# Kernel optimization log

Measured on AMD Instinct MI355X. Metric: run time of the kernel, lower is better.

Reference implementation:

```python
import jax, jax.numpy as jnp
import numpy as np

S, B, C, H, W_SP = 2, 16, 256, 64, 64
K = 3

def setup_inputs() -> dict:
    key = jax.random.key(0)
    k1, k2 = jax.random.split(key)
    x = jax.random.normal(k1, (S, B, C, H, W_SP), dtype=jnp.float32)
    W = jax.random.normal(k2, (C, C, K, K), dtype=jnp.float32) * 0.05
    return {"x": x, "W": W}

def reference(x, W):
    shape = x.shape
    C_ = shape[-3]
    k = W.shape[-1]
    pad = k // 2
    # flatten leading dims -> (N, C, H, W)
    xf = x.reshape((-1,) + shape[-3:])
    # diagonal mask: zero out all cross-channel filters (effectively depthwise)
    eye = jnp.eye(C_, dtype=W.dtype)[:, :, None, None]
    w = W * eye
    out = jax.lax.conv_general_dilated(
        xf, w,
        window_strides=(1, 1),
        padding=[(pad, pad), (pad, pad)],
        dimension_numbers=("NCHW", "OIHW", "NCHW"),
    )
    return out.reshape(shape)
```

## Files before the change

kernel.cpp:

```cpp
#include <hip/hip_runtime.h>


#define C_CH 256
#define H_SP 64
#define W_SP 64
#define PLANE (H_SP * W_SP)

__global__ __launch_bounds__(256) void dwconv3x3_kernel(
    const float* __restrict__ x,
    const float* __restrict__ Wfull,
    float* __restrict__ out)
{
    __shared__ float tile[PLANE];

    const int p = blockIdx.x;
    const int c = p & (C_CH - 1);
    const float* __restrict__ xp = x + (size_t)p * PLANE;
    float* __restrict__ op = out + (size_t)p * PLANE;

    const float* __restrict__ wp = Wfull + (size_t)c * (C_CH + 1) * 9;
    const float w00 = wp[0], w01 = wp[1], w02 = wp[2];
    const float w10 = wp[3], w11 = wp[4], w12 = wp[5];
    const float w20 = wp[6], w21 = wp[7], w22 = wp[8];

    const int t = threadIdx.x;

    const float4* __restrict__ xv = (const float4*)xp;
    float4* tv = (float4*)tile;
#pragma unroll
    for (int i = 0; i < 4; ++i) {
        tv[t + i * 256] = xv[t + i * 256];
    }
    __syncthreads();

#pragma unroll
    for (int i = 0; i < 4; ++i) {
        const int f  = t + i * 256;
        const int h  = f >> 4;
        const int w4 = (f & 15) << 2;

        float4 acc = make_float4(0.f, 0.f, 0.f, 0.f);

#pragma unroll
        for (int kh = 0; kh < 3; ++kh) {
            const int hh = h + kh - 1;
            if (hh < 0 || hh >= H_SP) continue;
            const float* row = &tile[hh * W_SP];

            const float cm1 = (w4 > 0)         ? row[w4 - 1] : 0.f;
            const float c0  = row[w4];
            const float c1  = row[w4 + 1];
            const float c2  = row[w4 + 2];
            const float c3  = row[w4 + 3];
            const float c4  = (w4 + 4 < W_SP)  ? row[w4 + 4] : 0.f;

            float k0, k1, k2;
            if (kh == 0)      { k0 = w00; k1 = w01; k2 = w02; }
            else if (kh == 1) { k0 = w10; k1 = w11; k2 = w12; }
            else              { k0 = w20; k1 = w21; k2 = w22; }

            acc.x += cm1 * k0 + c0 * k1 + c1 * k2;
            acc.y += c0  * k0 + c1 * k1 + c2 * k2;
            acc.z += c1  * k0 + c2 * k1 + c3 * k2;
            acc.w += c2  * k0 + c3 * k1 + c4 * k2;
        }

        ((float4*)op)[f] = acc;
    }
}

extern "C" void kernel_launch(void* const* d_in, const int* in_sizes, int n_in,
                              void* d_out, int out_size, void* d_ws, size_t ws_size,
                              hipStream_t stream) {
    const float* x = (const float*)d_in[0];
    const float* W = (const float*)d_in[1];
    float* out = (float*)d_out;

    const int n_planes = out_size / PLANE;
    dwconv3x3_kernel<<<n_planes, 256, 0, stream>>>(x, W, out);
}
```

Measured before the change: 229.9 us.

## Replace shared-memory tile with per-wavefront register sliding window and shuffles

Each wavefront now processes a whole plane: lanes own 4-column strips of 16 rows and slide a three-row register window down their rows, getting left and right halo values through lane shuffles instead of shared memory. This drops the 16KB LDS tile and the block barrier, which removes LDS traffic and raises occupancy. In exchange, rows at strip boundaries are reloaded from global memory (about 1.125x reads), and the loads are row-strided per lane rather than fully coalesced per block. The problem is memory-bound, so the gain depends on latency hiding.

```diff
diff --git a/kernel.cpp b/kernel.cpp
--- a/kernel.cpp
+++ b/kernel.cpp
@@ -6,66 +6,78 @@
 #define W_SP 64
 #define PLANE (H_SP * W_SP)
 
-__global__ __launch_bounds__(256) void dwconv3x3_kernel(
+__global__ __launch_bounds__(256, 4) void dwconv3x3_reg(
     const float* __restrict__ x,
     const float* __restrict__ Wfull,
     float* __restrict__ out)
 {
-    __shared__ float tile[PLANE];
+    const int tid  = threadIdx.x;
+    const int wid  = tid >> 6;
+    const int lane = tid & 63;
+    const int g    = lane >> 4;
+    const int cx   = lane & 15;
+    const int col0 = cx << 2;
+    const int r0   = g << 4;
 
-    const int p = blockIdx.x;
+    const int p = (blockIdx.x << 2) + wid;
     const int c = p & (C_CH - 1);
+
     const float* __restrict__ xp = x + (size_t)p * PLANE;
-    float* __restrict__ op = out + (size_t)p * PLANE;
+    float* __restrict__ op       = out + (size_t)p * PLANE;
 
     const float* __restrict__ wp = Wfull + (size_t)c * (C_CH + 1) * 9;
     const float w00 = wp[0], w01 = wp[1], w02 = wp[2];
     const float w10 = wp[3], w11 = wp[4], w12 = wp[5];
     const float w20 = wp[6], w21 = wp[7], w22 = wp[8];
 
-    const int t = threadIdx.x;
+    auto loadrow = [&](int h) -> float4 {
+        if (h >= 0 && h < H_SP)
+            return *(const float4*)(xp + h * W_SP + col0);
+        return make_float4(0.f, 0.f, 0.f, 0.f);
+    };
 
-    const float4* __restrict__ xv = (const float4*)xp;
-    float4* tv = (float4*)tile;
-#pragma unroll
-    for (int i = 0; i < 4; ++i) {
-        tv[t + i * 256] = xv[t + i * 256];
-    }
-    __syncthreads();
+    auto halo = [&](const float4& v, float& m, float& q) {
+        m = __shfl_up(v.w, 1);
+        q = __shfl_down(v.x, 1);
+        if (cx == 0)  m = 0.f;
+        if (cx == 15) q = 0.f;
+    };
+
+    float4 A, B, Cv, D = make_float4(0.f, 0.f, 0.f, 0.f);
+    float Am, Aq, Bm, Bq, Cm, Cq, Dm = 0.f, Dq = 0.f;
+
+    A  = loadrow(r0 - 1);
+    B  = loadrow(r0);
+    Cv = loadrow(r0 + 1);
+    halo(A, Am, Aq);
+    halo(B, Bm, Bq);
+    halo(Cv, Cm, Cq);
 
 #pragma unroll
-    for (int i = 0; i < 4; ++i) {
-        const int f  = t + i * 256;
-        const int h  = f >> 4;
-        const int w4 = (f & 15) << 2;
+    for (int s = 0; s < 16; ++s) {
+        if (s < 15) D = loadrow(r0 + s + 2);
 
-        float4 acc = make_float4(0.f, 0.f, 0.f, 0.f);
+        float4 acc;
+        acc.x = Am   * w00 + A.x  * w01 + A.y  * w02
+              + Bm   * w10 + B.x  * w11 + B.y  * w12
+              + Cm   * w20 + Cv.x * w21 + Cv.y * w22;
+        acc.y = A.x  * w00 + A.y  * w01 + A.z  * w02
+              + B.x  * w10 + B.y  * w11 + B.z  * w12
+              + Cv.x * w20 + Cv.y * w21 + Cv.z * w22;
+        acc.z = A.y  * w00 + A.z  * w01 + A.w  * w02
+              + B.y  * w10 + B.z  * w11 + B.w  * w12
+              + Cv.y * w20 + Cv.z * w21 + Cv.w * w22;
+        acc.w = A.z  * w00 + A.w  * w01 + Aq   * w02
+              + B.z  * w10 + B.w  * w11 + Bq   * w12
+              + Cv.z * w20 + Cv.w * w21 + Cq   * w22;
 
-#pragma unroll
-        for (int kh = 0; kh < 3; ++kh) {
-            const int hh = h + kh - 1;
-            if (hh < 0 || hh >= H_SP) continue;
-            const float* row = &tile[hh * W_SP];
+        *(float4*)(op + (r0 + s) * W_SP + col0) = acc;
 
-            const float cm1 = (w4 > 0)         ? row[w4 - 1] : 0.f;
-            const float c0  = row[w4];
-            const float c1  = row[w4 + 1];
-            const float c2  = row[w4 + 2];
-            const float c3  = row[w4 + 3];
-            const float c4  = (w4 + 4 < W_SP)  ? row[w4 + 4] : 0.f;
+        if (s < 15) halo(D, Dm, Dq);
 
-            float k0, k1, k2;
-            if (kh == 0)      { k0 = w00; k1 = w01; k2 = w02; }
-            else if (kh == 1) { k0 = w10; k1 = w11; k2 = w12; }
-            else              { k0 = w20; k1 = w21; k2 = w22; }
-
-            acc.x += cm1 * k0 + c0 * k1 + c1 * k2;
-            acc.y += c0  * k0 + c1 * k1 + c2 * k2;
-            acc.z += c1  * k0 + c2 * k1 + c3 * k2;
-            acc.w += c2  * k0 + c3 * k1 + c4 * k2;
-        }
-
-        ((float4*)op)[f] = acc;
+        A  = B;  Am = Bm; Aq = Bq;
+        B  = Cv; Bm = Cm; Bq = Cq;
+        Cv = D;  Cm = Dm; Cq = Dq;
     }
 }
 
@@ -77,5 +89,6 @@
     float* out = (float*)d_out;
 
     const int n_planes = out_size / PLANE;
-    dwconv3x3_kernel<<<n_planes, 256, 0, stream>>>(x, W, out);
+    const int n_blocks = n_planes >> 2;
+    dwconv3x3_reg<<<n_blocks, 256, 0, stream>>>(x, W, out);
 }
```

After: 265.7 us. 15.6% more time.
